# Performance work log

Measured on AMD Instinct MI355X. Metric: run time of the kernel, lower is better.

## Reference

```python
import jax, jax.numpy as jnp
import numpy as np

P = 7    # pool size (hard-coded in module)
DS = 16  # downsample rate


def _hat_int(t):
    # antiderivative of the bilinear hat kernel max(0, 1-|t|)
    t = jnp.clip(t, -1.0, 1.0)
    return jnp.where(t < 0, 0.5 * (t + 1.0) ** 2, 1.0 - 0.5 * (1.0 - t) ** 2)


def _axis_weights(lo, hi, size):
    # Exact per-pixel integration weights for PrRoIPool along one axis.
    # lo, hi: [R] scaled roi coords. Returns W [R,P,size], bin width [R].
    bw = (hi - lo) / P
    starts = lo[:, None] + bw[:, None] * jnp.arange(P, dtype=lo.dtype)  # [R,P]
    ends = starts + bw[:, None]
    idx = jnp.arange(size, dtype=lo.dtype)
    W = _hat_int(ends[:, :, None] - idx) - _hat_int(starts[:, :, None] - idx)
    return W, bw


def prroi_pool(feat, rois):
    # Precise RoI pooling: exact integral of the bilinearly-interpolated feature
    # over each bin (separable -> two small matmuls). feat [C,H,W], rois [R,4].
    C, H, Wd = feat.shape
    s = 1.0 / DS
    Wx, bw = _axis_weights(rois[:, 0] * s, rois[:, 2] * s, Wd)
    Wy, bh = _axis_weights(rois[:, 1] * s, rois[:, 3] * s, H)
    pooled = jnp.einsum('chw,rph,rqw->rcpq', feat, Wy, Wx)  # [R,C,P,P]
    area = jnp.maximum(bw * bh, 1e-8)
    return pooled / area[:, None, None, None]


def intersection_map(box1, box2):
    # Fractional coverage of each PxP bin of box2's grid by box1 -> [N,1,P,P]
    bw = (box2[:, 2] - box2[:, 0]) / P
    bh = (box2[:, 3] - box2[:, 1]) / P
    gx0 = box2[:, 0, None] + bw[:, None] * jnp.arange(P)
    gy0 = box2[:, 1, None] + bh[:, None] * jnp.arange(P)
    ox = jnp.clip(jnp.minimum(gx0 + bw[:, None], box1[:, 2, None]) - jnp.maximum(gx0, box1[:, 0, None]), 0.0)
    oy = jnp.clip(jnp.minimum(gy0 + bh[:, None], box1[:, 3, None]) - jnp.maximum(gy0, box1[:, 1, None]), 0.0)
    frac = oy[:, :, None] * ox[:, None, :] / jnp.maximum(bw * bh, 1e-8)[:, None, None]
    return frac[:, None]


def conv1x1(x, W, b):
    # 1x1 conv as a channel matmul; x [...,C,H,W], W [D,C], b [D]
    return jnp.einsum('...chw,dc->...dhw', x, W) + b[:, None, None]


def setup_inputs() -> dict:
    key = jax.random.key(0)
    ks = jax.random.split(key, 12)
    B, C, Hf, Wf, n = 8, 256, 32, 32, 16
    D1 = D2 = 256
    inp = jax.random.normal(ks[0], (B, C, Hf, Wf), dtype=jnp.float32)
    N = B * n
    xy1 = jax.random.uniform(ks[1], (N, 2), dtype=jnp.float32) * 380.0
    wh = 40.0 + jax.random.uniform(ks[2], (N, 2), dtype=jnp.float32) * 90.0
    objects = jnp.concatenate([xy1, xy1 + wh], axis=-1)  # valid boxes inside 512x512
    objects_length = jnp.full((B,), n, dtype=jnp.int32)

    def kaiming(k, shape, fan_in):
        return jax.random.normal(k, shape, dtype=jnp.float32) * np.float32(np.sqrt(2.0 / fan_in))

    rin = C // 2 * 3 + 2 * D1
    return {
        'input': inp, 'objects': objects, 'objects_length': objects_length,
        'Wc': kaiming(ks[3], (C, C), C), 'bc': jnp.zeros((C,), jnp.float32),
        'Wr': kaiming(ks[4], (C // 2 * 3, C), C), 'br': jnp.zeros((C // 2 * 3,), jnp.float32),
        'Wof': kaiming(ks[5], (D1, 2 * C), 2 * C), 'bof': jnp.zeros((D1,), jnp.float32),
        'Wrf': kaiming(ks[6], (D2, rin), rin), 'brf': jnp.zeros((D2,), jnp.float32),
        'Wofc': kaiming(ks[7], (D1, D1 * P * P), D1 * P * P), 'bofc': jnp.zeros((D1,), jnp.float32),
        'Wrfc': kaiming(ks[8], (D2, D2 * P * P), D2 * P * P), 'brfc': jnp.zeros((D2,), jnp.float32),
    }


def reference(input, objects, objects_length, Wc, bc, Wr, br, Wof, bof, Wrf, brf, Wofc, bofc, Wrfc, brfc):
    B, C, H, Wd = input.shape
    n = objects.shape[0] // B  # uniform object count per image
    boxes = objects.reshape(B, n, 4)
    ctx_all = conv1x1(input, Wc, bc)           # [B,C,H,W]
    rel_all = conv1x1(input, Wr, br)           # [B,3C/2,H,W]
    img_box = jnp.array([0.0, 0.0, Wd * DS, H * DS], dtype=input.dtype)
    sub_id = jnp.repeat(jnp.arange(n), n)
    obj_id = jnp.tile(jnp.arange(n), n)

    def per_image(feat, ctx, rel, box):
        # context pooled over the full-image box is identical for all objects
        ctx_pool = prroi_pool(ctx, img_box[None])[0]                    # [C,P,P]
        x_c, y_c = jnp.split(ctx_pool, 2, axis=0)
        box_imap = jax.lax.stop_gradient(
            intersection_map(box, jnp.broadcast_to(img_box, (n, 4))))  # [n,1,P,P]
        obj_pool = prroi_pool(feat, box)                                # [n,C,P,P]
        obj_in = jnp.concatenate([
            obj_pool,
            jnp.broadcast_to(x_c, (n,) + x_c.shape),
            y_c[None] * box_imap], axis=1)                              # [n,2C,P,P]
        obj_feat = conv1x1(obj_in, Wof, bof)                            # [n,D1,P,P]

        sub_box, ob_box = box[sub_id], box[obj_id]                      # [n*n,4]
        union = jax.lax.stop_gradient(jnp.concatenate(
            [jnp.minimum(sub_box[:, :2], ob_box[:, :2]),
             jnp.maximum(sub_box[:, 2:], ob_box[:, 2:])], axis=-1))
        sub_imap = jax.lax.stop_gradient(intersection_map(sub_box, union))
        obj_imap = jax.lax.stop_gradient(intersection_map(ob_box, union))
        rel_pool = prroi_pool(rel, union)                               # [n*n,3C/2,P,P]
        xr, yr, zr = jnp.split(rel_pool, 3, axis=1)
        rel_in = jnp.concatenate([
            obj_feat[sub_id], obj_feat[obj_id],
            xr, yr * sub_imap, zr * obj_imap], axis=1)                  # [n*n,2D1+3C/2,P,P]
        rel_feat = conv1x1(rel_in, Wrf, brf)                            # [n*n,D2,P,P]

        o = jax.nn.relu(obj_feat).reshape(n, -1) @ Wofc.T + bofc
        o = o / jnp.linalg.norm(o, axis=-1, keepdims=True)
        r = jax.nn.relu(rel_feat).reshape(n * n, -1) @ Wrfc.T + brfc
        r = r / jnp.linalg.norm(r, axis=-1, keepdims=True)
        return o, r.reshape(n, n, -1)

    obj_out, rel_out = jax.vmap(per_image)(input, ctx_all, rel_all, boxes)
    return obj_out, rel_out
```

## Files before the change

kernel.cpp:

```cpp
#include <hip/hip_runtime.h>
#include <hip/hip_bf16.h>


#define Bimg 8
#define Cch 256
#define HW 1024
#define CREL 384
#define CCAT 640
#define KFC 12544
#define STS 236

typedef __hip_bfloat16 bf16;
typedef __attribute__((ext_vector_type(8))) short short8;
typedef __attribute__((ext_vector_type(4))) short short4_t;
typedef __attribute__((ext_vector_type(4))) float f32x4;

__device__ __forceinline__ float hat_int(float t) {
    t = fminf(1.f, fmaxf(-1.f, t));
    return (t < 0.f) ? 0.5f * (t + 1.f) * (t + 1.f) : 1.f - 0.5f * (1.f - t) * (1.f - t);
}
__device__ __forceinline__ float b2f(short s) {
    return __uint_as_float(((unsigned)(unsigned short)s) << 16);
}

__global__ void prep_k(const float* __restrict__ Wc, const float* __restrict__ bc,
                       const float* __restrict__ Wr, const float* __restrict__ br,
                       bf16* __restrict__ Wcat, float* __restrict__ bcat,
                       const float* __restrict__ Wof, bf16* __restrict__ wof16,
                       const float* __restrict__ Wrf, bf16* __restrict__ wasao16,
                       bf16* __restrict__ wrfxyz16) {
    int bid = blockIdx.x, tid = threadIdx.x;
    if (bid < 640) {
        int t = bid * 256 + tid;
        int d = t >> 8, c = t & 255;
        Wcat[t] = __float2bfloat16((d < 256) ? Wc[d * 256 + c] : Wr[(d - 256) * 256 + c]);
        if (t < CCAT) bcat[t] = (t < 256) ? bc[t] : br[t - 256];
    } else if (bid < 1152) {
        int t = (bid - 640) * 256 + tid;
        wof16[t] = __float2bfloat16(Wof[t]);
    } else if (bid < 1664) {
        int t = (bid - 1152) * 256 + tid;
        int m = t >> 8, k = t & 255;
        wasao16[t] = __float2bfloat16((m < 256) ? Wrf[m * 896 + k] : Wrf[(m - 256) * 896 + 256 + k]);
    } else {
        int t = (bid - 1664) * 256 + tid;
        int d = t / 384, k = t - d * 384;
        wrfxyz16[t] = __float2bfloat16(Wrf[d * 896 + 512 + k]);
    }
}
__global__ __launch_bounds__(256) void wfc_pack_k(const float* __restrict__ W, bf16* __restrict__ dst) {
    __shared__ float ld[64 * 50];
    int dout = blockIdx.y, d0 = blockIdx.x * 64;
    int tid = threadIdx.x;
    for (int e = tid; e < 64 * 49; e += 256) {
        int di = e / 49, pq = e - di * 49;
        ld[di * 50 + pq] = W[(size_t)dout * KFC + (d0 + di) * 49 + pq];
    }
    __syncthreads();
    for (int e = tid; e < 64 * 49; e += 256) {
        int pq = e >> 6, di = e & 63;
        if (pq < 49)
            dst[(size_t)dout * KFC + pq * 256 + d0 + di] = __float2bfloat16(ld[di * 50 + pq]);
    }
}

__global__ void axisw_k(const float* __restrict__ objects,
                        float* __restrict__ orec, float* __restrict__ urec,
                        float* __restrict__ crec, float* __restrict__ bimap) {
    int bid = blockIdx.x;
    float b0, b1, b2, b3;
    float* rec;
    const float *sbp = nullptr, *obp = nullptr;
    if (bid < 128) {
        b0 = objects[bid * 4]; b1 = objects[bid * 4 + 1];
        b2 = objects[bid * 4 + 2]; b3 = objects[bid * 4 + 3];
        rec = orec + (size_t)bid * 128;
    } else if (bid < 2176) {
        int u = bid - 128;
        int img = u >> 8, pair = u & 255, i = pair >> 4, j = pair & 15;
        sbp = objects + (img * 16 + i) * 4;
        obp = objects + (img * 16 + j) * 4;
        b0 = fminf(sbp[0], obp[0]); b1 = fminf(sbp[1], obp[1]);
        b2 = fmaxf(sbp[2], obp[2]); b3 = fmaxf(sbp[3], obp[3]);
        rec = urec + (size_t)(u) * 224;
    } else {
        b0 = 0.f; b1 = 0.f; b2 = 512.f; b3 = 512.f;
        rec = crec;
    }
    const float sc = 0.0625f;
    float lox = b0 * sc, bwx = (b2 * sc - lox) * (1.f / 7.f);
    float loy = b1 * sc, bwy = (b3 * sc - loy) * (1.f / 7.f);
    float ia = 1.f / fmaxf(bwx * bwy, 1e-8f);
    int tid = threadIdx.x;
    if (tid < 56) {
        int p = tid >> 3, k = tid & 7;
        {
            float st = loy + bwy * p, en = st + bwy;
            int h0 = min(max((int)floorf(st) - 1, 0), 24);
            rec[tid] = hat_int(en - (float)(h0 + k)) - hat_int(st - (float)(h0 + k));
            if (k == 0) ((int*)rec)[119 + p] = h0;
        }
        {
            float st = lox + bwx * p, en = st + bwx;
            int w0 = min(max((int)floorf(st) - 1, 0), 24);
            rec[56 + tid] = ia * (hat_int(en - (float)(w0 + k)) - hat_int(st - (float)(w0 + k)));
            if (k == 0) ((int*)rec)[112 + p] = w0;
        }
    }
    if (tid < 49) {
        int p = tid / 7, q = tid - p * 7;
        if (bid < 128) {
            float bw = 512.f / 7.f, bh = 512.f / 7.f;
            float gx0 = bw * q, gy0 = bh * p;
            float ox = fmaxf(fminf(gx0 + bw, b2) - fmaxf(gx0, b0), 0.f);
            float oy = fmaxf(fminf(gy0 + bh, b3) - fmaxf(gy0, b1), 0.f);
            bimap[bid * 49 + tid] = oy * ox / fmaxf(bw * bh, 1e-8f);
        } else if (bid < 2176) {
            float bw = (b2 - b0) * (1.f / 7.f), bh = (b3 - b1) * (1.f / 7.f);
            float gx0 = b0 + bw * q, gy0 = b1 + bh * p;
            float inv = 1.f / fmaxf(bw * bh, 1e-8f);
            float oxs = fmaxf(fminf(gx0 + bw, sbp[2]) - fmaxf(gx0, sbp[0]), 0.f);
            float oys = fmaxf(fminf(gy0 + bh, sbp[3]) - fmaxf(gy0, sbp[1]), 0.f);
            rec[126 + tid] = oys * oxs * inv;
            float oxo = fmaxf(fminf(gx0 + bw, obp[2]) - fmaxf(gx0, obp[0]), 0.f);
            float oyo = fmaxf(fminf(gy0 + bh, obp[3]) - fmaxf(gy0, obp[1]), 0.f);
            rec[175 + tid] = oyo * oxo * inv;
        }
    }
}

__global__ __launch_bounds__(256) void int_t_k(const float* __restrict__ input, bf16* __restrict__ intp) {
    __shared__ float st[64][65];
    int hw0 = blockIdx.x * 64, c0 = blockIdx.y * 64, b = blockIdx.z;
    int tid = threadIdx.x;
#pragma unroll
    for (int i = 0; i < 16; i++) {
        int e = tid + i * 256;
        int c = e >> 6, hw = e & 63;
        st[c][hw] = input[(size_t)b * 262144 + (size_t)(c0 + c) * 1024 + hw0 + hw];
    }
    __syncthreads();
#pragma unroll
    for (int i = 0; i < 16; i++) {
        int e = tid + i * 256;
        int hw = e >> 6, c = e & 63;
        intp[((size_t)b * 1024 + hw0 + hw) * 256 + c0 + c] = __float2bfloat16(st[c][hw]);
    }
}

__global__ __launch_bounds__(256) void mfma_gemm_k(
    const bf16* __restrict__ A, int lda,
    const bf16* __restrict__ BT, int ldbt, long zB,
    int Ktiles, int splitk, int mode,
    float* __restrict__ Cf, int Mtot, int Ntot,
    const float* __restrict__ bias,
    const float* __restrict__ ASAOT, int bimg0,
    bf16* __restrict__ Ct, int ldct, long zC, bf16* __restrict__ Ct2) {
    __shared__ float tr[32 * 132];
    const int tid = threadIdx.x;
    const int m0 = blockIdx.y * 128, n0 = blockIdx.x * 128;
    int z = blockIdx.z;
    int kz = 0, bimg = bimg0;
    if (mode == 1) { BT += (size_t)z * zB; Ct += (size_t)z * zC; bimg = bimg0 + z; }
    else kz = z;
    const int tp = (Ktiles + splitk - 1) / splitk;
    const int kt0 = kz * tp;
    const int kt1 = min(Ktiles, kt0 + tp);
    const int lane = tid & 63, wid = tid >> 6;
    const int wm = (wid >> 1) * 64, wn = (wid & 1) * 64;
    const int lrow = lane & 15, lk = (lane >> 4) * 8;
    f32x4 acc[4][4];
#pragma unroll
    for (int i = 0; i < 4; i++)
#pragma unroll
        for (int j = 0; j < 4; j++) acc[i][j] = (f32x4){0.f, 0.f, 0.f, 0.f};
    const bf16* pA = A + (size_t)(m0 + wm + lrow) * lda + lk;
    const bf16* pB = BT + (size_t)(n0 + wn + lrow) * ldbt + lk;
    short8 a_c[4], b_c[4];
    if (kt0 < kt1) {
#pragma unroll
        for (int f = 0; f < 4; f++) {
            a_c[f] = *(const short8*)(pA + (size_t)f * 16 * lda + (size_t)kt0 * 32);
            b_c[f] = *(const short8*)(pB + (size_t)f * 16 * ldbt + (size_t)kt0 * 32);
        }
    }
    for (int kt = kt0; kt < kt1; kt++) {
        short8 a_n[4], b_n[4];
        if (kt + 1 < kt1) {
#pragma unroll
            for (int f = 0; f < 4; f++) {
                a_n[f] = *(const short8*)(pA + (size_t)f * 16 * lda + (size_t)(kt + 1) * 32);
                b_n[f] = *(const short8*)(pB + (size_t)f * 16 * ldbt + (size_t)(kt + 1) * 32);
            }
        }
#pragma unroll
        for (int i = 0; i < 4; i++)
#pragma unroll
            for (int j = 0; j < 4; j++)
                acc[i][j] = __builtin_amdgcn_mfma_f32_16x16x32_bf16(a_c[i], b_c[j], acc[i][j], 0, 0, 0);
#pragma unroll
        for (int f = 0; f < 4; f++) { a_c[f] = a_n[f]; b_c[f] = b_n[f]; }
    }
    const int rbase = (lane >> 4) * 4, cf = lane & 15;
    if (mode == 2) {
        float* P = Cf + (size_t)kz * Mtot * Ntot;
#pragma unroll
        for (int i = 0; i < 4; i++) {
            int mb = m0 + wm + i * 16 + rbase;
#pragma unroll
            for (int j = 0; j < 4; j++) {
                int n = n0 + wn + j * 16 + cf;
                *(f32x4*)&P[(size_t)n * Mtot + mb] = acc[i][j];
            }
        }
    } else if (mode == 3 || mode == 6) {
#pragma unroll
        for (int i = 0; i < 4; i++) {
            int mb = m0 + wm + i * 16 + rbase;
#pragma unroll
            for (int j = 0; j < 4; j++) {
                int n = n0 + wn + j * 16 + cf;
                short4_t pk, pr;
#pragma unroll
                for (int reg = 0; reg < 4; reg++) {
                    float v = acc[i][j][reg] + bias[mb + reg];
                    bf16 h = __float2bfloat16(v);
                    pk[reg] = *(short*)&h;
                    bf16 hr = __float2bfloat16(fmaxf(v, 0.f));
                    pr[reg] = *(short*)&hr;
                }
                *(short4_t*)&Ct[(size_t)n * ldct + mb] = pk;
                if (mode == 6) {
                    int r = n / 49, pq = n - r * 49;
                    *(short4_t*)&Ct2[(size_t)r * KFC + pq * 256 + mb] = pr;
                }
            }
        }
    } else if (mode == 4) {
#pragma unroll
        for (int i = 0; i < 4; i++) {
            int mb = m0 + wm + i * 16 + rbase;
#pragma unroll
            for (int j = 0; j < 4; j++) {
                int n = n0 + wn + j * 16 + cf;
                *(f32x4*)&Cf[(size_t)n * Mtot + mb] = acc[i][j];
            }
        }
    } else if (mode == 5) {
#pragma unroll
        for (int i = 0; i < 4; i++)
#pragma unroll
            for (int reg = 0; reg < 4; reg++) {
                int m = m0 + wm + i * 16 + rbase + reg;
                float bv = bias[m];
#pragma unroll
                for (int j = 0; j < 4; j++) {
                    int n = n0 + wn + j * 16 + cf;
                    Ct[(size_t)m * ldct + n] = __float2bfloat16(acc[i][j][reg] + bv);
                }
            }
    } else {
#pragma unroll 1
        for (int ci = 0; ci < 4; ci++) {
            __syncthreads();
            if ((wid & 1) == (ci >> 1)) {
                int jj0 = (ci & 1) * 2;
#pragma unroll
                for (int jj = jj0; jj < jj0 + 2; jj++)
#pragma unroll
                    for (int i = 0; i < 4; i++)
#pragma unroll
                        for (int reg = 0; reg < 4; reg++) {
                            int nl = (wn + jj * 16 + cf) - 32 * ci;
                            int ml = wm + i * 16 + rbase + reg;
                            tr[nl * 132 + ml] = acc[i][jj][reg];
                        }
            }
            __syncthreads();
            for (int e = tid; e < 32 * 128; e += 256) {
                int nl = e >> 7, ml = e & 127;
                int n = n0 + 32 * ci + nl;
                int m = m0 + ml;
                int r = n / 49, pq = n - r * 49;
                int ii = r >> 4, jj2 = r & 15;
                float v = tr[nl * 132 + ml] + bias[m]
                        + ASAOT[((size_t)bimg * 784 + ii * 49 + pq) * 512 + m]
                        + ASAOT[((size_t)bimg * 784 + jj2 * 49 + pq) * 512 + 256 + m];
                Ct[(size_t)r * KFC + pq * 256 + m] = __float2bfloat16(fmaxf(v, 0.f));
            }
        }
    }
}

__global__ __launch_bounds__(256) void objpool_k(
    const float* __restrict__ input, const float* __restrict__ orec,
    bf16* __restrict__ objint) {
    int cg = blockIdx.x;
    int b = blockIdx.y;
    __shared__ float sF[8192];
    __shared__ float sT[2][1888];
    __shared__ float wb[2][128];
    int tid = threadIdx.x;
    const float* feat = input + (size_t)b * (Cch * HW) + (size_t)cg * 8 * HW;
    for (int e4 = tid; e4 < 2048; e4 += 256)
        *(f32x4*)&sF[e4 * 4] = *(const f32x4*)&feat[e4 * 4];
    const float* rb = orec + (size_t)b * 16 * 128;
    if (tid < 126) wb[0][tid] = rb[tid];
    int t1v = tid + 256;
    int c0 = tid / 56, r0 = tid - c0 * 56, p0 = r0 >> 3, w40 = r0 & 7;
    int c1 = t1v / 56, r1 = t1v - c1 * 56, p1 = r1 >> 3, w41 = r1 & 7;
    bool has1 = (t1v < 448);
    int sf0 = c0 * 1024 + w40 * 4, st0 = c0 * STS + p0 * 32 + w40 * 4;
    int sf1 = c1 * 1024 + w41 * 4, st1 = c1 * STS + p1 * 32 + w41 * 4;
    int xpq0 = tid >> 3, xc = tid & 7;
    int xp0 = xpq0 / 7, xq0 = xpq0 - xp0 * 7;
    int xpq1 = xpq0 + 32;
    int xp1 = xpq1 / 7, xq1 = xpq1 - xp1 * 7;
    bool xv1 = (xpq1 < 49);
    __syncthreads();
    for (int r2 = 0; r2 < 16; r2++) {
        const float* wc_ = wb[r2 & 1];
        float* stbuf = sT[r2 & 1];
        float pre;
        bool pf = (r2 < 15) && (tid < 126);
        if (pf) pre = rb[(r2 + 1) * 128 + tid];
        {
            int h0 = ((const int*)wc_)[119 + p0];
            const f32x4* f = (const f32x4*)&sF[sf0 + h0 * 32];
            f32x4 wya = *(const f32x4*)&wc_[p0 * 8];
            f32x4 wyb = *(const f32x4*)&wc_[p0 * 8 + 4];
            f32x4 a = f[0] * wya[0] + f[8] * wya[1] + f[16] * wya[2] + f[24] * wya[3]
                    + f[32] * wyb[0] + f[40] * wyb[1] + f[48] * wyb[2] + f[56] * wyb[3];
            *(f32x4*)&stbuf[st0] = a;
        }
        if (has1) {
            int h0 = ((const int*)wc_)[119 + p1];
            const f32x4* f = (const f32x4*)&sF[sf1 + h0 * 32];
            f32x4 wya = *(const f32x4*)&wc_[p1 * 8];
            f32x4 wyb = *(const f32x4*)&wc_[p1 * 8 + 4];
            f32x4 a = f[0] * wya[0] + f[8] * wya[1] + f[16] * wya[2] + f[24] * wya[3]
                    + f[32] * wyb[0] + f[40] * wyb[1] + f[48] * wyb[2] + f[56] * wyb[3];
            *(f32x4*)&stbuf[st1] = a;
        }
        f32x4 xwa0 = *(const f32x4*)&wc_[56 + xq0 * 8];
        f32x4 xwb0 = *(const f32x4*)&wc_[56 + xq0 * 8 + 4];
        int w0i0 = ((const int*)wc_)[112 + xq0];
        f32x4 xwa1 = {0, 0, 0, 0}, xwb1 = {0, 0, 0, 0};
        int w0i1 = 0;
        if (xv1) {
            xwa1 = *(const f32x4*)&wc_[56 + xq1 * 8];
            xwb1 = *(const f32x4*)&wc_[56 + xq1 * 8 + 4];
            w0i1 = ((const int*)wc_)[112 + xq1];
        }
        if (pf) wb[1 - (r2 & 1)][tid] = pre;
        __syncthreads();
        {
            bf16* orow = objint + ((size_t)b * 784 + (size_t)r2 * 49) * 512 + cg * 8 + xc;
            {
                const float* t = &stbuf[xc * STS + xp0 * 32 + w0i0];
                float s = t[0] * xwa0[0] + t[1] * xwa0[1] + t[2] * xwa0[2] + t[3] * xwa0[3]
                        + t[4] * xwb0[0] + t[5] * xwb0[1] + t[6] * xwb0[2] + t[7] * xwb0[3];
                orow[(size_t)xpq0 * 512] = __float2bfloat16(s);
            }
            if (xv1) {
                const float* t = &stbuf[xc * STS + xp1 * 32 + w0i1];
                float s = t[0] * xwa1[0] + t[1] * xwa1[1] + t[2] * xwa1[2] + t[3] * xwa1[3]
                        + t[4] * xwb1[0] + t[5] * xwb1[1] + t[6] * xwb1[2] + t[7] * xwb1[3];
                orow[(size_t)xpq1 * 512] = __float2bfloat16(s);
            }
        }
    }
}

__global__ __launch_bounds__(256) void ctxobjin_k(
    const bf16* __restrict__ ctxrelb, const float* __restrict__ crec,
    const float* __restrict__ bimap, bf16* __restrict__ objint) {
    int cg = blockIdx.x;
    int b = blockIdx.y;
    __shared__ float sF[8192];
    __shared__ float sT[1888];
    __shared__ float wc_[128];
    __shared__ float sBI[784];
    int tid = threadIdx.x;
    for (int e4 = tid; e4 < 2048; e4 += 256) {
        short4_t v = *(const short4_t*)&ctxrelb[(size_t)(cg * 8 + (e4 >> 8)) * 8192 + b * 1024 + (e4 & 255) * 4];
        f32x4 fv = {b2f(v[0]), b2f(v[1]), b2f(v[2]), b2f(v[3])};
        *(f32x4*)&sF[e4 * 4] = fv;
    }
    if (tid < 126) wc_[tid] = crec[tid];
    for (int e = tid; e < 784; e += 256) sBI[e] = bimap[b * 784 + e];
    __syncthreads();
    for (int tt = tid; tt < 448; tt += 256) {
        int c = tt / 56, r = tt - c * 56, p = r >> 3, w4 = r & 7;
        int h0 = ((const int*)wc_)[119 + p];
        const f32x4* f = (const f32x4*)&sF[c * 1024 + w4 * 4 + h0 * 32];
        f32x4 wya = *(const f32x4*)&wc_[p * 8];
        f32x4 wyb = *(const f32x4*)&wc_[p * 8 + 4];
        f32x4 a = f[0] * wya[0] + f[8] * wya[1] + f[16] * wya[2] + f[24] * wya[3]
                + f[32] * wyb[0] + f[40] * wyb[1] + f[48] * wyb[2] + f[56] * wyb[3];
        *(f32x4*)&sT[c * STS + p * 32 + w4 * 4] = a;
    }
    __syncthreads();
    bool scale = (cg >= 16);
    for (int e = tid; e < 392; e += 256) {
        int pq = e >> 3, c = e & 7;
        int p = pq / 7, q = pq - p * 7;
        int w0i = ((const int*)wc_)[112 + q];
        const float* t = &sT[c * STS + p * 32 + w0i];
        const f32x4* wx4 = (const f32x4*)&wc_[56 + q * 8];
        f32x4 a = wx4[0], b2 = wx4[1];
        float s = t[0] * a[0] + t[1] * a[1] + t[2] * a[2] + t[3] * a[3]
                + t[4] * b2[0] + t[5] * b2[1] + t[6] * b2[2] + t[7] * b2[3];
        int j = cg * 8 + c;
        bf16* orow = objint + ((size_t)b * 784 + pq) * 512 + 256 + j;
#pragma unroll
        for (int r = 0; r < 16; r++) {
            float m = scale ? sBI[r * 49 + pq] : 1.f;
            orow[(size_t)r * 49 * 512] = __float2bfloat16(s * m);
        }
    }
}

__global__ __launch_bounds__(256) void relpool_k(
    const bf16* __restrict__ ctxrelb, const float* __restrict__ urec,
    bf16* __restrict__ mbt, int b0) {
    int cg = blockIdx.x;
    int rg = blockIdx.y;
    int zi = blockIdx.z;
    int b = b0 + zi;
    mbt += (size_t)zi * 4816896;
    __shared__ float sF[8192];
    __shared__ float sT[2][1888];
    __shared__ float wb[2][224];
    int tid = threadIdx.x;
    for (int e4 = tid; e4 < 2048; e4 += 256) {
        short4_t v = *(const short4_t*)&ctxrelb[(size_t)(256 + cg * 8 + (e4 >> 8)) * 8192 + b * 1024 + (e4 & 255) * 4];
        f32x4 fv = {b2f(v[0]), b2f(v[1]), b2f(v[2]), b2f(v[3])};
        *(f32x4*)&sF[e4 * 4] = fv;
    }
    const float* rb = urec + ((size_t)b * 256 + (size_t)rg * 16) * 224;
    if (tid < 224) wb[0][tid] = rb[tid];
    int t1v = tid + 256;
    int c0 = tid / 56, r0 = tid - c0 * 56, p0 = r0 >> 3, w40 = r0 & 7;
    int c1 = t1v / 56, r1 = t1v - c1 * 56, p1 = r1 >> 3, w41 = r1 & 7;
    bool has1 = (t1v < 448);
    int sf0 = c0 * 1024 + w40 * 4, st0 = c0 * STS + p0 * 32 + w40 * 4;
    int sf1 = c1 * 1024 + w41 * 4, st1 = c1 * STS + p1 * 32 + w41 * 4;
    int xpq0 = tid >> 3, xc = tid & 7;
    int xp0 = xpq0 / 7, xq0 = xpq0 - xp0 * 7;
    int xpq1 = xpq0 + 32;
    int xp1 = xpq1 / 7, xq1 = xpq1 - xp1 * 7;
    bool xv1 = (xpq1 < 49);
    int cglob = cg * 8 + xc;
    int mclass = (cglob >= 256) ? 2 : (cglob >= 128 ? 1 : 0);
    __syncthreads();
    for (int r2 = 0; r2 < 16; r2++) {
        const float* wc_ = wb[r2 & 1];
        float* stbuf = sT[r2 & 1];
        float pre;
        bool pf = (r2 < 15) && (tid < 224);
        if (pf) pre = rb[(r2 + 1) * 224 + tid];
        {
            int h0 = ((const int*)wc_)[119 + p0];
            const f32x4* f = (const f32x4*)&sF[sf0 + h0 * 32];
            f32x4 wya = *(const f32x4*)&wc_[p0 * 8];
            f32x4 wyb = *(const f32x4*)&wc_[p0 * 8 + 4];
            f32x4 a = f[0] * wya[0] + f[8] * wya[1] + f[16] * wya[2] + f[24] * wya[3]
                    + f[32] * wyb[0] + f[40] * wyb[1] + f[48] * wyb[2] + f[56] * wyb[3];
            *(f32x4*)&stbuf[st0] = a;
        }
        if (has1) {
            int h0 = ((const int*)wc_)[119 + p1];
            const f32x4* f = (const f32x4*)&sF[sf1 + h0 * 32];
            f32x4 wya = *(const f32x4*)&wc_[p1 * 8];
            f32x4 wyb = *(const f32x4*)&wc_[p1 * 8 + 4];
            f32x4 a = f[0] * wya[0] + f[8] * wya[1] + f[16] * wya[2] + f[24] * wya[3]
                    + f[32] * wyb[0] + f[40] * wyb[1] + f[48] * wyb[2] + f[56] * wyb[3];
            *(f32x4*)&stbuf[st1] = a;
        }
        f32x4 xwa0 = *(const f32x4*)&wc_[56 + xq0 * 8];
        f32x4 xwb0 = *(const f32x4*)&wc_[56 + xq0 * 8 + 4];
        int w0i0 = ((const int*)wc_)[112 + xq0];
        float mul0 = (mclass == 2) ? wc_[175 + xpq0] : (mclass == 1 ? wc_[126 + xpq0] : 1.f);
        f32x4 xwa1 = {0, 0, 0, 0}, xwb1 = {0, 0, 0, 0};
        int w0i1 = 0;
        float mul1 = 1.f;
        if (xv1) {
            xwa1 = *(const f32x4*)&wc_[56 + xq1 * 8];
            xwb1 = *(const f32x4*)&wc_[56 + xq1 * 8 + 4];
            w0i1 = ((const int*)wc_)[112 + xq1];
            mul1 = (mclass == 2) ? wc_[175 + xpq1] : (mclass == 1 ? wc_[126 + xpq1] : 1.f);
        }
        if (pf) wb[1 - (r2 & 1)][tid] = pre;
        __syncthreads();
        {
            int r = rg * 16 + r2;
            bf16* orow = mbt + (size_t)r * 49 * 384 + cglob;
            {
                const float* t = &stbuf[xc * STS + xp0 * 32 + w0i0];
                float s = t[0] * xwa0[0] + t[1] * xwa0[1] + t[2] * xwa0[2] + t[3] * xwa0[3]
                        + t[4] * xwb0[0] + t[5] * xwb0[1] + t[6] * xwb0[2] + t[7] * xwb0[3];
                orow[(size_t)xpq0 * 384] = __float2bfloat16(s * mul0);
            }
            if (xv1) {
                const float* t = &stbuf[xc * STS + xp1 * 32 + w0i1];
                float s = t[0] * xwa1[0] + t[1] * xwa1[1] + t[2] * xwa1[2] + t[3] * xwa1[3]
                        + t[4] * xwb1[0] + t[5] * xwb1[1] + t[6] * xwb1[2] + t[7] * xwb1[3];
                orow[(size_t)xpq1 * 384] = __float2bfloat16(s * mul1);
            }
        }
    }
}

__global__ void redns_k(const float* __restrict__ Pd, const float* __restrict__ bias,
                        float* __restrict__ out, int N, int splitk, long outBase) {
    int vec = blockIdx.x, m = threadIdx.x;
    float s = bias[m];
    for (int z = 0; z < splitk; z++) s += Pd[(size_t)z * 256 * N + (size_t)vec * 256 + m];
    float ss = s * s;
    for (int o = 32; o > 0; o >>= 1) ss += __shfl_down(ss, o, 64);
    __shared__ float red[4];
    if ((m & 63) == 0) red[m >> 6] = ss;
    __syncthreads();
    float tot = red[0] + red[1] + red[2] + red[3];
    out[outBase + (size_t)vec * 256 + m] = s / sqrtf(tot);
}

extern "C" void kernel_launch(void* const* d_in, const int* in_sizes, int n_in,
                              void* d_out, int out_size, void* d_ws, size_t ws_size,
                              hipStream_t stream) {
    const float* input = (const float*)d_in[0];
    const float* objects = (const float*)d_in[1];
    const float* Wc = (const float*)d_in[3];
    const float* bc = (const float*)d_in[4];
    const float* Wr = (const float*)d_in[5];
    const float* br = (const float*)d_in[6];
    const float* Wof = (const float*)d_in[7];
    const float* bof = (const float*)d_in[8];
    const float* Wrf = (const float*)d_in[9];
    const float* brf = (const float*)d_in[10];
    const float* Wofc = (const float*)d_in[11];
    const float* bofc = (const float*)d_in[12];
    const float* Wrfc = (const float*)d_in[13];
    const float* brfc = (const float*)d_in[14];
    float* out = (float*)d_out;

    float* w = (float*)d_ws;
    bf16* WCAT16   = (bf16*)(w + 0);
    float* BCAT    = w + 81920;
    bf16* CTXRELB  = (bf16*)(w + 82560);
    float* OREC    = w + 2704000;
    float* UREC    = w + 2720384;
    float* CREC    = w + 3179136;
    float* BIMAP   = w + 3179264;
    float* ASAOT   = w + 3185536;
    bf16* WRFXYZ16 = (bf16*)(w + 6396800);
    bf16* WRFC16   = (bf16*)(w + 6445952);
    float* OVL     = w + 8051584;
    bf16* INT16    = (bf16*)(OVL + 0);
    bf16* WOF16    = (bf16*)(OVL + 1048576);
    bf16* WASAO16  = (bf16*)(OVL + 1114112);
    bf16* WOFC16   = (bf16*)(OVL + 1179648);
    bf16* OBJINT   = (bf16*)(OVL + 2885632);
    bf16* OBJFT    = (bf16*)(OVL + 4491264);
    bf16* XOT      = (bf16*)(OVL + 5294080);
    float* OPART   = OVL + 6096896;
    bf16* MBT2     = (bf16*)(OVL + 0);
    bf16* XBT2     = (bf16*)(OVL + 4816896);
    float* RPART   = OVL + 8028160;

    prep_k<<<dim3(2048), 256, 0, stream>>>(Wc, bc, Wr, br, WCAT16, BCAT,
                                           Wof, WOF16, Wrf, WASAO16, WRFXYZ16);
    wfc_pack_k<<<dim3(4, 256), 256, 0, stream>>>(Wrfc, WRFC16);
    wfc_pack_k<<<dim3(4, 256), 256, 0, stream>>>(Wofc, WOFC16);
    axisw_k<<<dim3(2177), 64, 0, stream>>>(objects, OREC, UREC, CREC, BIMAP);
    int_t_k<<<dim3(16, 4, 8), 256, 0, stream>>>(input, INT16);
    mfma_gemm_k<<<dim3(64, 5, 1), 256, 0, stream>>>(WCAT16, 256, INT16, 256, 0L, 8, 1, 5,
                                                    nullptr, 640, 8192, BCAT,
                                                    nullptr, 0, CTXRELB, 8192, 0L, nullptr);
    objpool_k<<<dim3(32, 8), 256, 0, stream>>>(input, OREC, OBJINT);
    ctxobjin_k<<<dim3(32, 8), 256, 0, stream>>>(CTXRELB, CREC, BIMAP, OBJINT);
    mfma_gemm_k<<<dim3(49, 2, 1), 256, 0, stream>>>(WOF16, 512, OBJINT, 512, 0L, 16, 1, 6,
                                                    nullptr, 256, 6272, bof,
                                                    nullptr, 0, OBJFT, 256, 0L, XOT);
    mfma_gemm_k<<<dim3(49, 4, 1), 256, 0, stream>>>(WASAO16, 256, OBJFT, 256, 0L, 8, 1, 4,
                                                    ASAOT, 512, 6272, nullptr,
                                                    nullptr, 0, nullptr, 0, 0L, nullptr);
    mfma_gemm_k<<<dim3(1, 2, 56), 256, 0, stream>>>(WOFC16, KFC, XOT, KFC, 0L, 392, 56, 2,
                                                    OPART, 256, 128, nullptr,
                                                    nullptr, 0, nullptr, 0, 0L, nullptr);
    redns_k<<<dim3(128), 256, 0, stream>>>(OPART, bofc, out, 128, 56, 0L);

    for (int g = 0; g < 4; g++) {
        int b0 = g * 2;
        relpool_k<<<dim3(48, 16, 2), 256, 0, stream>>>(CTXRELB, UREC, MBT2, b0);
        mfma_gemm_k<<<dim3(98, 2, 2), 256, 0, stream>>>(WRFXYZ16, 384, MBT2, 384, 4816896L,
                                                        12, 1, 1,
                                                        nullptr, 256, KFC, brf,
                                                        ASAOT, b0, XBT2, 0, 3211264L, nullptr);
        mfma_gemm_k<<<dim3(4, 2, 24), 256, 0, stream>>>(WRFC16, KFC, XBT2, KFC, 0L, 392, 24, 2,
                                                        RPART, 256, 512, nullptr,
                                                        nullptr, 0, nullptr, 0, 0L, nullptr);
        redns_k<<<dim3(512), 256, 0, stream>>>(RPART, brfc, out, 512, 24,
                                               32768L + (long)g * 131072L);
    }
}
```

Measured before the change: 741.8 us.

## Store ASAOT in bf16 and process relation stage in groups of four images

The sub/obj projection GEMM now writes its output as bf16 through the existing bias/bf16 epilogue instead of fp32, halving the ASAOT footprint and the bytes gathered in the relation GEMM epilogue. The freed workspace is used to rebuild the buffer layout so the relation pipeline (pooling, conv GEMM, FC split-K GEMM, reduction) runs two groups of four images instead of four groups of two. This halves the kernel launches and gives each launch a larger grid for better occupancy. The cost is extra bf16 rounding on the ASAOT additive terms and a larger working set per group.

```diff
diff --git a/kernel.cpp b/kernel.cpp
--- a/kernel.cpp
+++ b/kernel.cpp
@@ -154,7 +154,7 @@
     int Ktiles, int splitk, int mode,
     float* __restrict__ Cf, int Mtot, int Ntot,
     const float* __restrict__ bias,
-    const float* __restrict__ ASAOT, int bimg0,
+    const bf16* __restrict__ ASAOT, int bimg0,
     bf16* __restrict__ Ct, int ldct, long zC, bf16* __restrict__ Ct2) {
     __shared__ float tr[32 * 132];
     const int tid = threadIdx.x;
@@ -223,7 +223,7 @@
                 short4_t pk, pr;
 #pragma unroll
                 for (int reg = 0; reg < 4; reg++) {
-                    float v = acc[i][j][reg] + bias[mb + reg];
+                    float v = acc[i][j][reg] + (bias ? bias[mb + reg] : 0.f);
                     bf16 h = __float2bfloat16(v);
                     pk[reg] = *(short*)&h;
                     bf16 hr = __float2bfloat16(fmaxf(v, 0.f));
@@ -236,16 +236,6 @@
                 }
             }
         }
-    } else if (mode == 4) {
-#pragma unroll
-        for (int i = 0; i < 4; i++) {
-            int mb = m0 + wm + i * 16 + rbase;
-#pragma unroll
-            for (int j = 0; j < 4; j++) {
-                int n = n0 + wn + j * 16 + cf;
-                *(f32x4*)&Cf[(size_t)n * Mtot + mb] = acc[i][j];
-            }
-        }
     } else if (mode == 5) {
 #pragma unroll
         for (int i = 0; i < 4; i++)
@@ -283,9 +273,9 @@
                 int m = m0 + ml;
                 int r = n / 49, pq = n - r * 49;
                 int ii = r >> 4, jj2 = r & 15;
-                float v = tr[nl * 132 + ml] + bias[m]
-                        + ASAOT[((size_t)bimg * 784 + ii * 49 + pq) * 512 + m]
-                        + ASAOT[((size_t)bimg * 784 + jj2 * 49 + pq) * 512 + 256 + m];
+                float as = b2f(*(const short*)&ASAOT[((size_t)bimg * 784 + ii * 49 + pq) * 512 + m]);
+                float ao = b2f(*(const short*)&ASAOT[((size_t)bimg * 784 + jj2 * 49 + pq) * 512 + 256 + m]);
+                float v = tr[nl * 132 + ml] + bias[m] + as + ao;
                 Ct[(size_t)r * KFC + pq * 256 + m] = __float2bfloat16(fmaxf(v, 0.f));
             }
         }
@@ -553,21 +543,21 @@
     float* UREC    = w + 2720384;
     float* CREC    = w + 3179136;
     float* BIMAP   = w + 3179264;
-    float* ASAOT   = w + 3185536;
-    bf16* WRFXYZ16 = (bf16*)(w + 6396800);
-    bf16* WRFC16   = (bf16*)(w + 6445952);
-    float* OVL     = w + 8051584;
+    bf16* ASAOT16  = (bf16*)(w + 3185536);
+    bf16* WRFXYZ16 = (bf16*)(w + 4791168);
+    bf16* WRFC16   = (bf16*)(w + 4840320);
+    float* OVL     = w + 6445952;
     bf16* INT16    = (bf16*)(OVL + 0);
     bf16* WOF16    = (bf16*)(OVL + 1048576);
     bf16* WASAO16  = (bf16*)(OVL + 1114112);
     bf16* WOFC16   = (bf16*)(OVL + 1179648);
-    bf16* OBJINT   = (bf16*)(OVL + 2885632);
-    bf16* OBJFT    = (bf16*)(OVL + 4491264);
-    bf16* XOT      = (bf16*)(OVL + 5294080);
-    float* OPART   = OVL + 6096896;
-    bf16* MBT2     = (bf16*)(OVL + 0);
-    bf16* XBT2     = (bf16*)(OVL + 4816896);
-    float* RPART   = OVL + 8028160;
+    bf16* OBJINT   = (bf16*)(OVL + 2785280);
+    bf16* OBJFT    = (bf16*)(OVL + 4390912);
+    bf16* XOT      = (bf16*)(OVL + 5193728);
+    float* OPART   = OVL + 5996544;
+    bf16* MBT4     = (bf16*)(OVL + 0);
+    float* RPART   = OVL + 0;
+    bf16* XBT4     = (bf16*)(OVL + 9633792);
 
     prep_k<<<dim3(2048), 256, 0, stream>>>(Wc, bc, Wr, br, WCAT16, BCAT,
                                            Wof, WOF16, Wrf, WASAO16, WRFXYZ16);
@@ -583,25 +573,25 @@
     mfma_gemm_k<<<dim3(49, 2, 1), 256, 0, stream>>>(WOF16, 512, OBJINT, 512, 0L, 16, 1, 6,
                                                     nullptr, 256, 6272, bof,
                                                     nullptr, 0, OBJFT, 256, 0L, XOT);
-    mfma_gemm_k<<<dim3(49, 4, 1), 256, 0, stream>>>(WASAO16, 256, OBJFT, 256, 0L, 8, 1, 4,
-                                                    ASAOT, 512, 6272, nullptr,
-                                                    nullptr, 0, nullptr, 0, 0L, nullptr);
+    mfma_gemm_k<<<dim3(49, 4, 1), 256, 0, stream>>>(WASAO16, 256, OBJFT, 256, 0L, 8, 1, 3,
+                                                    nullptr, 512, 6272, nullptr,
+                                                    nullptr, 0, ASAOT16, 512, 0L, nullptr);
     mfma_gemm_k<<<dim3(1, 2, 56), 256, 0, stream>>>(WOFC16, KFC, XOT, KFC, 0L, 392, 56, 2,
                                                     OPART, 256, 128, nullptr,
                                                     nullptr, 0, nullptr, 0, 0L, nullptr);
     redns_k<<<dim3(128), 256, 0, stream>>>(OPART, bofc, out, 128, 56, 0L);
 
-    for (int g = 0; g < 4; g++) {
-        int b0 = g * 2;
-        relpool_k<<<dim3(48, 16, 2), 256, 0, stream>>>(CTXRELB, UREC, MBT2, b0);
-        mfma_gemm_k<<<dim3(98, 2, 2), 256, 0, stream>>>(WRFXYZ16, 384, MBT2, 384, 4816896L,
+    for (int g = 0; g < 2; g++) {
+        int b0 = g * 4;
+        relpool_k<<<dim3(48, 16, 4), 256, 0, stream>>>(CTXRELB, UREC, MBT4, b0);
+        mfma_gemm_k<<<dim3(98, 2, 4), 256, 0, stream>>>(WRFXYZ16, 384, MBT4, 384, 4816896L,
                                                         12, 1, 1,
                                                         nullptr, 256, KFC, brf,
-                                                        ASAOT, b0, XBT2, 0, 3211264L, nullptr);
-        mfma_gemm_k<<<dim3(4, 2, 24), 256, 0, stream>>>(WRFC16, KFC, XBT2, KFC, 0L, 392, 24, 2,
-                                                        RPART, 256, 512, nullptr,
+                                                        ASAOT16, b0, XBT4, 0, 3211264L, nullptr);
+        mfma_gemm_k<<<dim3(8, 2, 24), 256, 0, stream>>>(WRFC16, KFC, XBT4, KFC, 0L, 392, 24, 2,
+                                                        RPART, 256, 1024, nullptr,
                                                         nullptr, 0, nullptr, 0, 0L, nullptr);
-        redns_k<<<dim3(512), 256, 0, stream>>>(RPART, brfc, out, 512, 24,
-                                               32768L + (long)g * 131072L);
-    }
-}
+        redns_k<<<dim3(1024), 256, 0, stream>>>(RPART, brfc, out, 1024, 24,
+                                                32768L + (long)g * 262144L);
+    }
+}
```

Result: faster. 691.6 us (-6.8%).
